# Kernel tuning notes

Hardware: AMD Instinct MI355X
Metric: run time of the kernel (lower is better)

The kernel has to match this reference:

```python
import jax, jax.numpy as jnp
import numpy as np

N_NODES = 100000
IN_CH = 256
HIDDEN = 256
N_EDGES = 500000


def setup_inputs() -> dict:
    key = jax.random.key(0)
    k_emb, k_ei, k_w1, k_w2 = jax.random.split(key, 4)
    embeddings = jax.random.normal(k_emb, (N_NODES, IN_CH), dtype=jnp.float32)
    edge_index = jax.random.randint(k_ei, (2, N_EDGES), 0, N_NODES, dtype=jnp.int64)
    # Linear(in*2, hidden) and Linear(hidden, 1) weights (stored input-major for x @ W)
    s1 = 1.0 / np.sqrt(2 * IN_CH)
    s2 = 1.0 / np.sqrt(HIDDEN)
    W1 = jax.random.uniform(k_w1, (2 * IN_CH, HIDDEN), dtype=jnp.float32, minval=-s1, maxval=s1)
    b1 = jnp.zeros((HIDDEN,), dtype=jnp.float32)
    W2 = jax.random.uniform(k_w2, (HIDDEN, 1), dtype=jnp.float32, minval=-s2, maxval=s2)
    b2 = jnp.zeros((1,), dtype=jnp.float32)
    return {"embeddings": embeddings, "edge_index": edge_index,
            "W1": W1, "b1": b1, "W2": W2, "b2": b2}


def reference(embeddings, edge_index, W1, b1, W2, b2):
    src, dst = edge_index[0], edge_index[1]
    # gather [E, in] twice, concat -> [E, 2*in]
    feats = jnp.concatenate([embeddings[src], embeddings[dst]], axis=-1)
    h = jax.nn.relu(feats @ W1 + b1)          # [E, hidden]
    scores = h @ W2 + b2                      # [E, 1]
    return scores.reshape(-1)
```

## Files before the change

kernel.cpp:

```cpp
#include <hip/hip_runtime.h>
#include <hip/hip_bf16.h>

#define NN   100000
#define EE   500000
#define MPAD 100096

using bf16x8 = __attribute__((ext_vector_type(8))) short;
using f32x4  = __attribute__((ext_vector_type(4))) float;
using u16x8  = __attribute__((ext_vector_type(8))) unsigned short;

__device__ __forceinline__ unsigned short f2bf(float f) {
  unsigned int x = __builtin_bit_cast(unsigned int, f);
  x += 0x7fffu + ((x >> 16) & 1u);
  return (unsigned short)(x >> 16);
}
__device__ __forceinline__ float bf2f(unsigned short u) {
  unsigned int x = ((unsigned int)u) << 16;
  return __builtin_bit_cast(float, x);
}
__device__ __forceinline__ unsigned short f2bh(float f) {
  return __builtin_bit_cast(unsigned short, __float2bfloat16(f));
}

__global__ void wprep_kernel(const float* __restrict__ W1, unsigned short* __restrict__ WT) {
  int id = blockIdx.x * blockDim.x + threadIdx.x;
  if (id >= 512 * 32) return;
  int j  = id >> 5;
  int cg = id & 31;
  int jc = j & 255;
  int kb = (cg << 3) + ((j >= 256) ? 256 : 0);
  u16x8 v;
#pragma unroll
  for (int t = 0; t < 8; ++t)
    v[t] = f2bf(W1[(size_t)(kb + t) * 256 + jc]);
  *reinterpret_cast<u16x8*>(WT + (size_t)j * 256 + (cg << 3)) = v;
}

__global__ __launch_bounds__(256, 2) void gemm_pq(const float* __restrict__ emb,
                                                  const unsigned short* __restrict__ WT,
                                                  const float* __restrict__ b1,
                                                  unsigned short* __restrict__ R) {
  __shared__ unsigned short ldsA[8][128 * 32];

  const int t    = threadIdx.x;
  const int lane = t & 63;
  const int wave = t >> 6;
  const int wrow = wave >> 1, wcol = wave & 1;
  const int bid = (int)blockIdx.x;
  const int lid = (bid & 7) * 391 + (bid >> 3);
  const int m0 = (lid >> 2) * 128;
  const int n0 = (lid & 3) * 128;

  const int a_r = t >> 1, a_h = t & 1;
  int arow_g = m0 + a_r; if (arow_g >= NN) arow_g = NN - 1;
  const float* aSrc = emb + (size_t)arow_g * 256 + (a_h << 4);
  const int swzA = (a_r >> 1) & 3;
  const int aW0  = a_r * 32 + ((((a_h << 1) | 0) ^ swzA) << 3);
  const int aW1  = a_r * 32 + ((((a_h << 1) | 1) ^ swzA) << 3);
#pragma unroll
  for (int s = 0; s < 8; ++s) {
    float4 f0 = *(const float4*)(aSrc + s * 32);
    float4 f1 = *(const float4*)(aSrc + s * 32 + 4);
    float4 f2 = *(const float4*)(aSrc + s * 32 + 8);
    float4 f3 = *(const float4*)(aSrc + s * 32 + 12);
    u16x8 w0, w1;
    w0[0] = f2bh(f0.x); w0[1] = f2bh(f0.y); w0[2] = f2bh(f0.z); w0[3] = f2bh(f0.w);
    w0[4] = f2bh(f1.x); w0[5] = f2bh(f1.y); w0[6] = f2bh(f1.z); w0[7] = f2bh(f1.w);
    w1[0] = f2bh(f2.x); w1[1] = f2bh(f2.y); w1[2] = f2bh(f2.z); w1[3] = f2bh(f2.w);
    w1[4] = f2bh(f3.x); w1[5] = f2bh(f3.y); w1[6] = f2bh(f3.z); w1[7] = f2bh(f3.w);
    *(u16x8*)&ldsA[s][aW0] = w0;
    *(u16x8*)&ldsA[s][aW1] = w1;
  }

  const int fr = lane & 15, fq = lane >> 4;
  int aoff[4];
#pragma unroll
  for (int m = 0; m < 4; ++m) {
    const int r = wrow * 64 + 16 * m + fr;
    aoff[m] = r * 32 + ((fq ^ ((r >> 1) & 3)) << 3);
  }
  const unsigned short* bRow[4];
#pragma unroll
  for (int n = 0; n < 4; ++n)
    bRow[n] = WT + (size_t)(n0 + wcol * 64 + 16 * n + fr) * 256 + (fq << 3);

  bf16x8 bv[4][4];
#pragma unroll
  for (int s = 0; s < 4; ++s)
#pragma unroll
    for (int n = 0; n < 4; ++n)
      bv[s][n] = *(const bf16x8*)(bRow[n] + (s << 5));

  __syncthreads();

  f32x4 acc[4][4] = {};
  bf16x8 av[2][4];
#pragma unroll
  for (int m = 0; m < 4; ++m) av[0][m] = *(const bf16x8*)&ldsA[0][aoff[m]];

#pragma unroll
  for (int ks = 0; ks < 8; ++ks) {
    const int cur = ks & 1;
    if (ks < 7) {
#pragma unroll
      for (int m = 0; m < 4; ++m)
        av[cur ^ 1][m] = *(const bf16x8*)&ldsA[ks + 1][aoff[m]];
    }
#pragma unroll
    for (int m = 0; m < 4; ++m)
#pragma unroll
      for (int n = 0; n < 4; ++n)
        acc[m][n] = __builtin_amdgcn_mfma_f32_16x16x32_bf16(av[cur][m], bv[ks & 3][n],
                                                            acc[m][n], 0, 0, 0);
    if (ks < 4) {
#pragma unroll
      for (int n = 0; n < 4; ++n)
        bv[ks & 3][n] = *(const bf16x8*)(bRow[n] + ((ks + 4) << 5));
    }
  }

  float bn[4];
#pragma unroll
  for (int n = 0; n < 4; ++n) {
    const int c = n0 + wcol * 64 + 16 * n + fr;
    bn[n] = (c < 256) ? b1[c] : 0.f;
  }
#pragma unroll
  for (int m = 0; m < 4; ++m) {
    const int r0 = m0 + wrow * 64 + 16 * m + (fq << 2);
#pragma unroll
    for (int n = 0; n < 4; ++n) {
      const int c = n0 + wcol * 64 + 16 * n + fr;
#pragma unroll
      for (int i = 0; i < 4; ++i)
        R[(size_t)(r0 + i) * 512 + c] = f2bh(acc[m][n][i] + bn[n]);
    }
  }
}

__global__ __launch_bounds__(256) void edge_kernel(const int* __restrict__ idx,
                                                   const unsigned short* __restrict__ R,
                                                   const float* __restrict__ W2,
                                                   const float* __restrict__ b2,
                                                   float* __restrict__ out) {
  const int lane  = threadIdx.x & 63;
  const int half  = lane >> 5;
  const int l     = lane & 31;
  const int gwave = (int)((blockIdx.x * blockDim.x + threadIdx.x) >> 6);
  const int nwave = (int)((gridDim.x * blockDim.x) >> 6);
  const float4 w0 = *(const float4*)(W2 + (l << 3));
  const float4 w1 = *(const float4*)(W2 + (l << 3) + 4);
  const float bias = b2[0];

  for (int c = gwave; c < (EE / 8); c += nwave) {
    const int e0 = c << 3;
    int s[4], d[4];
#pragma unroll
    for (int u = 0; u < 4; ++u) {
      s[u] = idx[e0 + (u << 1) + half];
      d[u] = idx[EE + e0 + (u << 1) + half];
    }
    u16x8 ga[4], gb[4];
#pragma unroll
    for (int u = 0; u < 4; ++u) {
      ga[u] = *(const u16x8*)(R + (size_t)s[u] * 512 + (l << 3));
      gb[u] = *(const u16x8*)(R + (size_t)d[u] * 512 + 256 + (l << 3));
    }
#pragma unroll
    for (int u = 0; u < 4; ++u) {
      float acc;
      acc  = fmaxf(bf2f((unsigned short)ga[u][0]) + bf2f((unsigned short)gb[u][0]), 0.f) * w0.x;
      acc += fmaxf(bf2f((unsigned short)ga[u][1]) + bf2f((unsigned short)gb[u][1]), 0.f) * w0.y;
      acc += fmaxf(bf2f((unsigned short)ga[u][2]) + bf2f((unsigned short)gb[u][2]), 0.f) * w0.z;
      acc += fmaxf(bf2f((unsigned short)ga[u][3]) + bf2f((unsigned short)gb[u][3]), 0.f) * w0.w;
      acc += fmaxf(bf2f((unsigned short)ga[u][4]) + bf2f((unsigned short)gb[u][4]), 0.f) * w1.x;
      acc += fmaxf(bf2f((unsigned short)ga[u][5]) + bf2f((unsigned short)gb[u][5]), 0.f) * w1.y;
      acc += fmaxf(bf2f((unsigned short)ga[u][6]) + bf2f((unsigned short)gb[u][6]), 0.f) * w1.z;
      acc += fmaxf(bf2f((unsigned short)ga[u][7]) + bf2f((unsigned short)gb[u][7]), 0.f) * w1.w;
#pragma unroll
      for (int off = 16; off > 0; off >>= 1) acc += __shfl_xor(acc, off, 64);
      if (l == 0) out[e0 + (u << 1) + half] = acc + bias;
    }
  }
}

__global__ __launch_bounds__(256) void fallback_kernel(const float* __restrict__ emb,
                                                       const int* __restrict__ idx,
                                                       const float* __restrict__ W1,
                                                       const float* __restrict__ b1,
                                                       const float* __restrict__ W2,
                                                       const float* __restrict__ b2,
                                                       float* __restrict__ out) {
  __shared__ float feats[512];
  __shared__ float red[256];
  const int t = threadIdx.x;
  for (int e = blockIdx.x; e < EE; e += gridDim.x) {
    __syncthreads();
    const int s = idx[e], d = idx[EE + e];
    feats[t]       = emb[(size_t)s * 256 + t];
    feats[256 + t] = emb[(size_t)d * 256 + t];
    __syncthreads();
    float h = b1[t];
    for (int k = 0; k < 512; ++k) h += feats[k] * W1[k * 256 + t];
    red[t] = fmaxf(h, 0.f) * W2[t];
    __syncthreads();
    for (int off = 128; off > 0; off >>= 1) {
      if (t < off) red[t] += red[t + off];
      __syncthreads();
    }
    if (t == 0) out[e] = red[0] + b2[0];
  }
}

extern "C" void kernel_launch(void* const* d_in, const int* in_sizes, int n_in,
                              void* d_out, int out_size, void* d_ws, size_t ws_size,
                              hipStream_t stream) {
  const float* emb = (const float*)d_in[0];
  const int*   idx = (const int*)d_in[1];
  const float* W1  = (const float*)d_in[2];
  const float* b1  = (const float*)d_in[3];
  const float* W2  = (const float*)d_in[4];
  const float* b2  = (const float*)d_in[5];
  float* out = (float*)d_out;

  const size_t wt_elems = (size_t)512 * 256;
  const size_t r_elems  = (size_t)MPAD * 512;
  const size_t need = (wt_elems + r_elems) * sizeof(unsigned short);

  if (ws_size < need) {
    fallback_kernel<<<4096, 256, 0, stream>>>(emb, idx, W1, b1, W2, b2, out);
    return;
  }

  unsigned short* WT = (unsigned short*)d_ws;
  unsigned short* R  = WT + wt_elems;

  wprep_kernel<<<64, 256, 0, stream>>>(W1, WT);
  gemm_pq<<<(MPAD / 128) * 4, 256, 0, stream>>>(emb, WT, b1, R);
  edge_kernel<<<2048, 256, 0, stream>>>(idx, R, W2, b2, out);
}
```

Measured before the change: 162.5 us.

## Rewrite node GEMM as persistent kernel with register-resident weights and prefetched A strips

The node projection GEMM becomes a persistent kernel of 256 blocks with 8 waves each. Every wave keeps its 64-column slice of the bf16 weight matrix in registers for the whole run and loops over 16-row strips of the embeddings. The next strip's fp32 rows are prefetched into registers while the current strip's MFMAs run. LDS staging and the 4x re-reading of each embedding tile across column blocks go away, so embeddings are read once. In exchange register use is heavy (128 VGPRs for B plus prefetch), occupancy is limited, and the output stores are narrow 2-byte scattered writes.

```diff
diff --git a/kernel.cpp b/kernel.cpp
--- a/kernel.cpp
+++ b/kernel.cpp
@@ -4,6 +4,7 @@
 #define NN   100000
 #define EE   500000
 #define MPAD 100096
+#define NSTRIP 6256
 
 using bf16x8 = __attribute__((ext_vector_type(8))) short;
 using f32x4  = __attribute__((ext_vector_type(4))) float;
@@ -36,106 +37,95 @@
   *reinterpret_cast<u16x8*>(WT + (size_t)j * 256 + (cg << 3)) = v;
 }
 
-__global__ __launch_bounds__(256, 2) void gemm_pq(const float* __restrict__ emb,
-                                                  const unsigned short* __restrict__ WT,
-                                                  const float* __restrict__ b1,
-                                                  unsigned short* __restrict__ R) {
-  __shared__ unsigned short ldsA[8][128 * 32];
-
+__global__ __launch_bounds__(512) void gemm_pq(const float* __restrict__ emb,
+                                               const unsigned short* __restrict__ WT,
+                                               const float* __restrict__ b1,
+                                               unsigned short* __restrict__ R) {
   const int t    = threadIdx.x;
   const int lane = t & 63;
   const int wave = t >> 6;
-  const int wrow = wave >> 1, wcol = wave & 1;
-  const int bid = (int)blockIdx.x;
-  const int lid = (bid & 7) * 391 + (bid >> 3);
-  const int m0 = (lid >> 2) * 128;
-  const int n0 = (lid & 3) * 128;
-
-  const int a_r = t >> 1, a_h = t & 1;
-  int arow_g = m0 + a_r; if (arow_g >= NN) arow_g = NN - 1;
-  const float* aSrc = emb + (size_t)arow_g * 256 + (a_h << 4);
-  const int swzA = (a_r >> 1) & 3;
-  const int aW0  = a_r * 32 + ((((a_h << 1) | 0) ^ swzA) << 3);
-  const int aW1  = a_r * 32 + ((((a_h << 1) | 1) ^ swzA) << 3);
-#pragma unroll
-  for (int s = 0; s < 8; ++s) {
-    float4 f0 = *(const float4*)(aSrc + s * 32);
-    float4 f1 = *(const float4*)(aSrc + s * 32 + 4);
-    float4 f2 = *(const float4*)(aSrc + s * 32 + 8);
-    float4 f3 = *(const float4*)(aSrc + s * 32 + 12);
-    u16x8 w0, w1;
-    w0[0] = f2bh(f0.x); w0[1] = f2bh(f0.y); w0[2] = f2bh(f0.z); w0[3] = f2bh(f0.w);
-    w0[4] = f2bh(f1.x); w0[5] = f2bh(f1.y); w0[6] = f2bh(f1.z); w0[7] = f2bh(f1.w);
-    w1[0] = f2bh(f2.x); w1[1] = f2bh(f2.y); w1[2] = f2bh(f2.z); w1[3] = f2bh(f2.w);
-    w1[4] = f2bh(f3.x); w1[5] = f2bh(f3.y); w1[6] = f2bh(f3.z); w1[7] = f2bh(f3.w);
-    *(u16x8*)&ldsA[s][aW0] = w0;
-    *(u16x8*)&ldsA[s][aW1] = w1;
-  }
-
-  const int fr = lane & 15, fq = lane >> 4;
-  int aoff[4];
-#pragma unroll
-  for (int m = 0; m < 4; ++m) {
-    const int r = wrow * 64 + 16 * m + fr;
-    aoff[m] = r * 32 + ((fq ^ ((r >> 1) & 3)) << 3);
-  }
-  const unsigned short* bRow[4];
-#pragma unroll
-  for (int n = 0; n < 4; ++n)
-    bRow[n] = WT + (size_t)(n0 + wcol * 64 + 16 * n + fr) * 256 + (fq << 3);
-
-  bf16x8 bv[4][4];
-#pragma unroll
-  for (int s = 0; s < 4; ++s)
+  const int fr   = lane & 15, fq = lane >> 4;
+
+  bf16x8 B[8][4];
+  {
+    const unsigned short* wb = WT + (size_t)(wave * 64 + fr) * 256 + (fq << 3);
 #pragma unroll
     for (int n = 0; n < 4; ++n)
-      bv[s][n] = *(const bf16x8*)(bRow[n] + (s << 5));
-
-  __syncthreads();
-
-  f32x4 acc[4][4] = {};
-  bf16x8 av[2][4];
-#pragma unroll
-  for (int m = 0; m < 4; ++m) av[0][m] = *(const bf16x8*)&ldsA[0][aoff[m]];
-
-#pragma unroll
-  for (int ks = 0; ks < 8; ++ks) {
-    const int cur = ks & 1;
-    if (ks < 7) {
-#pragma unroll
-      for (int m = 0; m < 4; ++m)
-        av[cur ^ 1][m] = *(const bf16x8*)&ldsA[ks + 1][aoff[m]];
-    }
-#pragma unroll
-    for (int m = 0; m < 4; ++m)
-#pragma unroll
-      for (int n = 0; n < 4; ++n)
-        acc[m][n] = __builtin_amdgcn_mfma_f32_16x16x32_bf16(av[cur][m], bv[ks & 3][n],
-                                                            acc[m][n], 0, 0, 0);
-    if (ks < 4) {
-#pragma unroll
-      for (int n = 0; n < 4; ++n)
-        bv[ks & 3][n] = *(const bf16x8*)(bRow[n] + ((ks + 4) << 5));
-    }
-  }
-
+#pragma unroll
+      for (int ks = 0; ks < 8; ++ks)
+        B[ks][n] = *(const bf16x8*)(wb + n * 4096 + ks * 32);
+  }
   float bn[4];
 #pragma unroll
   for (int n = 0; n < 4; ++n) {
-    const int c = n0 + wcol * 64 + 16 * n + fr;
+    const int c = wave * 64 + 16 * n + fr;
     bn[n] = (c < 256) ? b1[c] : 0.f;
   }
-#pragma unroll
-  for (int m = 0; m < 4; ++m) {
-    const int r0 = m0 + wrow * 64 + 16 * m + (fq << 2);
-#pragma unroll
-    for (int n = 0; n < 4; ++n) {
-      const int c = n0 + wcol * 64 + 16 * n + fr;
-#pragma unroll
-      for (int i = 0; i < 4; ++i)
-        R[(size_t)(r0 + i) * 512 + c] = f2bh(acc[m][n][i] + bn[n]);
-    }
-  }
+
+  float4 lo0, hi0, lo1, hi1, lo2, hi2, lo3, hi3;
+  float4 lo4, hi4, lo5, hi5, lo6, hi6, lo7, hi7;
+
+#define AREF(ptr, k, LO, HI)                                                   \
+  do { LO = *(const float4*)((ptr) + (k) * 32);                                \
+       HI = *(const float4*)((ptr) + (k) * 32 + 4); } while (0)
+
+#define CONS(ks, LO, HI)                                                       \
+  do {                                                                         \
+    bf16x8 av;                                                                 \
+    av[0] = (short)f2bh(LO.x); av[1] = (short)f2bh(LO.y);                      \
+    av[2] = (short)f2bh(LO.z); av[3] = (short)f2bh(LO.w);                      \
+    av[4] = (short)f2bh(HI.x); av[5] = (short)f2bh(HI.y);                      \
+    av[6] = (short)f2bh(HI.z); av[7] = (short)f2bh(HI.w);                      \
+    a0 = __builtin_amdgcn_mfma_f32_16x16x32_bf16(av, B[ks][0], a0, 0, 0, 0);   \
+    a1 = __builtin_amdgcn_mfma_f32_16x16x32_bf16(av, B[ks][1], a1, 0, 0, 0);   \
+    a2 = __builtin_amdgcn_mfma_f32_16x16x32_bf16(av, B[ks][2], a2, 0, 0, 0);   \
+    a3 = __builtin_amdgcn_mfma_f32_16x16x32_bf16(av, B[ks][3], a3, 0, 0, 0);   \
+  } while (0)
+
+  int s = blockIdx.x;
+  const float* ap;
+  {
+    int ar = s * 16 + fr; if (ar >= NN) ar = NN - 1;
+    ap = emb + (size_t)ar * 256 + (fq << 3);
+  }
+  AREF(ap, 0, lo0, hi0); AREF(ap, 1, lo1, hi1);
+  AREF(ap, 2, lo2, hi2); AREF(ap, 3, lo3, hi3);
+  AREF(ap, 4, lo4, hi4); AREF(ap, 5, lo5, hi5);
+  AREF(ap, 6, lo6, hi6); AREF(ap, 7, lo7, hi7);
+
+  while (s < NSTRIP) {
+    const int sn = s + 256;
+    const bool more = (sn < NSTRIP);
+    const float* apn;
+    {
+      int ar = (more ? sn : s) * 16 + fr; if (ar >= NN) ar = NN - 1;
+      apn = emb + (size_t)ar * 256 + (fq << 3);
+    }
+    f32x4 a0 = {0.f, 0.f, 0.f, 0.f}, a1 = a0, a2 = a0, a3 = a0;
+
+    CONS(0, lo0, hi0); if (more) AREF(apn, 0, lo0, hi0);
+    CONS(1, lo1, hi1); if (more) AREF(apn, 1, lo1, hi1);
+    CONS(2, lo2, hi2); if (more) AREF(apn, 2, lo2, hi2);
+    CONS(3, lo3, hi3); if (more) AREF(apn, 3, lo3, hi3);
+    CONS(4, lo4, hi4); if (more) AREF(apn, 4, lo4, hi4);
+    CONS(5, lo5, hi5); if (more) AREF(apn, 5, lo5, hi5);
+    CONS(6, lo6, hi6); if (more) AREF(apn, 6, lo6, hi6);
+    CONS(7, lo7, hi7); if (more) AREF(apn, 7, lo7, hi7);
+
+    unsigned short* rp = R + (size_t)(s * 16) * 512 + wave * 64;
+#pragma unroll
+    for (int i = 0; i < 4; ++i) {
+      const size_t ro = (size_t)(fq * 4 + i) * 512;
+      rp[ro + fr]      = f2bh(a0[i] + bn[0]);
+      rp[ro + 16 + fr] = f2bh(a1[i] + bn[1]);
+      rp[ro + 32 + fr] = f2bh(a2[i] + bn[2]);
+      rp[ro + 48 + fr] = f2bh(a3[i] + bn[3]);
+    }
+    ap = apn;
+    s = sn;
+  }
+#undef AREF
+#undef CONS
 }
 
 __global__ __launch_bounds__(256) void edge_kernel(const int* __restrict__ idx,
@@ -236,6 +226,6 @@
   unsigned short* R  = WT + wt_elems;
 
   wprep_kernel<<<64, 256, 0, stream>>>(W1, WT);
-  gemm_pq<<<(MPAD / 128) * 4, 256, 0, stream>>>(emb, WT, b1, R);
+  gemm_pq<<<256, 512, 0, stream>>>(emb, WT, b1, R);
   edge_kernel<<<2048, 256, 0, stream>>>(idx, R, W2, b2, out);
 }
```

Result: slower. 189.3 us (+16.5%).
